# Optimization experiments

Measured on AMD Instinct MI355X. Metric: run time of the kernel, lower is better.

## Reference

```python
import jax, jax.numpy as jnp
import numpy as np

BN_EPS = 1e-5
LEAKY_SLOPE = 0.2


def setup_inputs() -> dict:
    key = jax.random.key(0)
    k1, k2 = jax.random.split(key, 2)
    B, C, N, O, K = 8, 64, 4096, 64, 20
    x = jax.random.normal(k1, (B, C, N), dtype=jnp.float32)
    W = jax.random.normal(k2, (O, 2 * C), dtype=jnp.float32) * 0.05  # 1x1 conv weight
    gamma = jnp.ones((O,), dtype=jnp.float32)
    beta = jnp.zeros((O,), dtype=jnp.float32)
    return {"x": x, "W": W, "gamma": gamma, "beta": beta, "k": K}


def reference(x, W, gamma, beta, k):
    # x: (B, C, N)
    xt = jnp.transpose(x, (0, 2, 1))  # (B, N, C)
    # kNN via squared euclidean distances (same ordering as cdist p=2)
    sq = jnp.sum(xt * xt, axis=-1)  # (B, N)
    d2 = sq[:, :, None] + sq[:, None, :] - 2.0 * jnp.einsum('bnc,bmc->bnm', xt, xt)
    idx = jax.lax.top_k(-d2, k)[1]  # (B, N, k) nearest neighbors (incl. self)
    # gather neighbor features: (B, N, k, C)
    xj = jax.vmap(lambda f, i: f[i])(xt, idx)
    xi = xt[:, :, None, :]  # (B, N, 1, C)
    edge = jnp.concatenate([xj - xi, jnp.broadcast_to(xi, xj.shape)], axis=-1)  # (B, N, k, 2C)
    # 1x1 conv == channel GEMM
    h = jnp.einsum('bnkc,oc->bnko', edge, W)  # (B, N, k, O)
    # BatchNorm2d, training-mode batch statistics over (B, N, k) per channel
    mean = jnp.mean(h, axis=(0, 1, 2))
    var = jnp.mean(jnp.square(h - mean), axis=(0, 1, 2))
    hn = (h - mean) * jax.lax.rsqrt(var + BN_EPS) * gamma + beta
    # LeakyReLU(0.2); dropout omitted (eval / identity)
    act = jnp.where(hn >= 0, hn, LEAKY_SLOPE * hn)
    # max over the k neighbors -> (B, N, O) -> (B, O, N)
    out = jnp.max(act, axis=2)
    return jnp.transpose(out, (0, 2, 1))
```

## Files before the change

### kernel.cpp

```cpp
#include <hip/hip_runtime.h>
#include <math.h>

#define Bn 8
#define Cc 64
#define Nn 4096
#define Oo 64
#define Kk 20
#define Kh 10
#define QCAP 16
#define NTOT (Bn*Nn*Kk)

typedef __attribute__((ext_vector_type(8))) short short8;
typedef __attribute__((ext_vector_type(4))) float f32x4;

__device__ __forceinline__ unsigned bf16_rn(float v) {
  unsigned u = __float_as_uint(v);
  return (u + 0x7FFFu + ((u >> 16) & 1)) >> 16;
}

__global__ __launch_bounds__(256) void k_split(const float* __restrict__ x,
                                               unsigned short* __restrict__ xs3,
                                               float* __restrict__ sqv) {
  __shared__ float xs[64][68];
  int tid = threadIdx.x;
  int b = blockIdx.x & 7;
  int n0 = (blockIdx.x >> 3) << 6;
  for (int i = 0; i < 4; i++) {
    int c = i * 16 + (tid >> 4);
    int n = (tid & 15) * 4;
    float4 v = *(const float4*)&x[((size_t)b * Cc + c) * Nn + n0 + n];
    *(float4*)&xs[c][n] = v;
  }
  __syncthreads();
  for (int i = 0; i < 4; i++) {
    int n = i * 16 + (tid >> 4);
    int c = (tid & 15) * 4;
    ushort4 h4, m4, l4;
    unsigned short* hp = (unsigned short*)&h4;
    unsigned short* mp = (unsigned short*)&m4;
    unsigned short* lp = (unsigned short*)&l4;
#pragma unroll
    for (int j = 0; j < 4; j++) {
      float v = xs[c + j][n];
      unsigned hb = bf16_rn(v);
      float hf = __uint_as_float(hb << 16);
      float r1 = v - hf;
      unsigned mb = bf16_rn(r1);
      float mf = __uint_as_float(mb << 16);
      float r2 = r1 - mf;
      unsigned lb = bf16_rn(r2);
      hp[j] = (unsigned short)hb;
      mp[j] = (unsigned short)mb;
      lp[j] = (unsigned short)lb;
    }
    size_t o = ((size_t)(b << 12) + n0 + n) * 192 + c;
    *(ushort4*)&xs3[o] = h4;
    *(ushort4*)&xs3[o + 64] = m4;
    *(ushort4*)&xs3[o + 128] = l4;
  }
  if (tid < 64) {
    float s = 0.f;
#pragma unroll
    for (int c = 0; c < 64; c++) { float v = xs[c][tid]; s = fmaf(v, v, s); }
    sqv[b * Nn + n0 + tid] = s;
  }
}

__global__ __launch_bounds__(256) void k_y1z(const float* __restrict__ x,
                                             const float* __restrict__ Wm,
                                             float* __restrict__ y1,
                                             float* __restrict__ z) {
  __shared__ float xs[64][68];
  __shared__ float Wl[64][129];
  int tid = threadIdx.x;
  int b = blockIdx.x & 7;
  int n0 = (blockIdx.x >> 3) << 6;
  for (int i = tid; i < 64 * 128; i += 256) Wl[i >> 7][i & 127] = Wm[i];
  for (int i = 0; i < 4; i++) {
    int c = i * 16 + (tid >> 4);
    int n = (tid & 15) * 4;
    float4 v = *(const float4*)&x[((size_t)b * Cc + c) * Nn + n0 + n];
    *(float4*)&xs[c][n] = v;
  }
  __syncthreads();
  int o = tid & 63, ng = tid >> 6;
  for (int p = 0; p < 4; p++) {
    int nb = p * 16 + ng * 4;
    float a1[4] = {0.f, 0.f, 0.f, 0.f};
    float a2[4] = {0.f, 0.f, 0.f, 0.f};
#pragma unroll 8
    for (int c = 0; c < 64; c++) {
      float4 xv = *(const float4*)&xs[c][nb];
      float w1v = Wl[o][c], w2v = Wl[o][64 + c];
      float xa[4] = {xv.x, xv.y, xv.z, xv.w};
#pragma unroll
      for (int j = 0; j < 4; j++) {
        a1[j] = fmaf(xa[j], w1v, a1[j]);
        a2[j] = fmaf(xa[j], w2v, a2[j]);
      }
    }
#pragma unroll
    for (int j = 0; j < 4; j++) {
      size_t off = ((size_t)b * Nn + n0 + nb + j) * 64 + o;
      y1[off] = a1[j];
      z[off] = a2[j] - a1[j];
    }
  }
}

__global__ __launch_bounds__(512, 4) void k_knn(const unsigned short* __restrict__ xs3,
                                                const float* __restrict__ sqv,
                                                int* __restrict__ idxout) {
  __shared__ alignas(16) short Bs[2][3][64][72];
  __shared__ float thrS[2][64];
  __shared__ float sqs[2][64];
  __shared__ alignas(16) float qk[2][64][20];
  __shared__ alignas(16) unsigned short qm[2][64][24];
  __shared__ int qcnt[2][64];

  const int tid = threadIdx.x;
  const int lane = tid & 63;
  const int w = tid >> 6;
  const int grp = w >> 2;
  const int wg = w & 3;
  const int tig = tid & 255;
  const int b = blockIdx.x & 7;
  const int n0 = (blockIdx.x >> 3) << 6;
  const int lm = lane & 15;
  const int q = lane >> 4;
  const bool handler = (lane < 32);
  const int hrow = wg * 16 + (lane >> 1);
  const bool isL = (lane & 1) == 0;

  float hk[Kh];
  int hix[Kh];
#pragma unroll
  for (int kk = 0; kk < Kh; kk++) { hk[kk] = INFINITY; hix[kk] = 0; }

  if (handler && !isL) { thrS[grp][hrow] = INFINITY; qcnt[grp][hrow] = 0; }

  const size_t arow = ((size_t)(b << 12) + n0 + wg * 16 + lm) * 192;
  short8 ah0 = *(const short8*)&xs3[arow + q * 8];
  short8 ah1 = *(const short8*)&xs3[arow + 32 + q * 8];
  short8 am0 = *(const short8*)&xs3[arow + 64 + q * 8];
  short8 am1 = *(const short8*)&xs3[arow + 96 + q * 8];
  short8 al0 = *(const short8*)&xs3[arow + 128 + q * 8];
  short8 al1 = *(const short8*)&xs3[arow + 160 + q * 8];

  const unsigned short* gp = xs3 + ((size_t)(b << 12) + grp * 2048) * 192 + tig * 8;
  short* ld[6];
#pragma unroll
  for (int i = 0; i < 6; i++) {
    int f = i * 256 + tig;
    int r = f / 24;
    int rem = f - r * 24;
    int layer = rem >> 3;
    int qq = rem & 7;
    ld[i] = &Bs[grp][layer][r][qq * 8];
  }

  f32x4 acc[4];

  for (int t = 0; t < 32; t++) {
    const int m0 = grp * 2048 + t * 64;
    __syncthreads();
#pragma unroll
    for (int i = 0; i < 6; i++) {
      short8 v = *(const short8*)(gp + i * 2048);
      *(short8*)ld[i] = v;
    }
    gp += 12288;
    if (tig < 16) ((float4*)sqs[grp])[tig] = ((const float4*)(sqv + b * Nn + m0))[tig];
    __syncthreads();

#pragma unroll
    for (int g = 0; g < 4; g++) {
      const int mr = g * 16 + lm;
      short8 bh0 = *(const short8*)&Bs[grp][0][mr][q * 8];
      short8 bh1 = *(const short8*)&Bs[grp][0][mr][32 + q * 8];
      short8 bm0 = *(const short8*)&Bs[grp][1][mr][q * 8];
      short8 bm1 = *(const short8*)&Bs[grp][1][mr][32 + q * 8];
      short8 bl0 = *(const short8*)&Bs[grp][2][mr][q * 8];
      short8 bl1 = *(const short8*)&Bs[grp][2][mr][32 + q * 8];
      f32x4 a = (f32x4){0.f, 0.f, 0.f, 0.f};
      a = __builtin_amdgcn_mfma_f32_16x16x32_bf16(am0, bm0, a, 0, 0, 0);
      a = __builtin_amdgcn_mfma_f32_16x16x32_bf16(am1, bm1, a, 0, 0, 0);
      a = __builtin_amdgcn_mfma_f32_16x16x32_bf16(ah0, bl0, a, 0, 0, 0);
      a = __builtin_amdgcn_mfma_f32_16x16x32_bf16(ah1, bl1, a, 0, 0, 0);
      a = __builtin_amdgcn_mfma_f32_16x16x32_bf16(al0, bh0, a, 0, 0, 0);
      a = __builtin_amdgcn_mfma_f32_16x16x32_bf16(al1, bh1, a, 0, 0, 0);
      a = __builtin_amdgcn_mfma_f32_16x16x32_bf16(ah0, bm0, a, 0, 0, 0);
      a = __builtin_amdgcn_mfma_f32_16x16x32_bf16(ah1, bm1, a, 0, 0, 0);
      a = __builtin_amdgcn_mfma_f32_16x16x32_bf16(am0, bh0, a, 0, 0, 0);
      a = __builtin_amdgcn_mfma_f32_16x16x32_bf16(am1, bh1, a, 0, 0, 0);
      a = __builtin_amdgcn_mfma_f32_16x16x32_bf16(ah0, bh0, a, 0, 0, 0);
      a = __builtin_amdgcn_mfma_f32_16x16x32_bf16(ah1, bh1, a, 0, 0, 0);
      acc[g] = a;
    }

    unsigned pend = 0;
    {
      float tl[4];
#pragma unroll
      for (int r = 0; r < 4; r++) tl[r] = thrS[grp][wg * 16 + q * 4 + r];
#pragma unroll
      for (int g = 0; g < 4; g++) {
        float sv = sqs[grp][g * 16 + lm];
#pragma unroll
        for (int r = 0; r < 4; r++) {
          float key = fmaf(-2.f, acc[g][r], sv);
          acc[g][r] = key;
          if (key < tl[r]) pend |= 1u << (g * 4 + r);
        }
      }
    }

    for (;;) {
      if (pend) {
#pragma unroll
        for (int g = 0; g < 4; g++) {
#pragma unroll
          for (int r = 0; r < 4; r++) {
            unsigned bit = 1u << (g * 4 + r);
            if (pend & bit) {
              int row = wg * 16 + q * 4 + r;
              int p = atomicAdd(&qcnt[grp][row], 1);
              if (p < QCAP) {
                qk[grp][row][p] = acc[g][r];
                qm[grp][row][p] = (unsigned short)(m0 + g * 16 + lm);
                pend &= ~bit;
              }
            }
          }
        }
      }
      unsigned long long anyovf = __ballot(pend != 0);

      if (handler) {
        int cn = qcnt[grp][hrow];
        if (cn > QCAP) cn = QCAP;
        for (int p0 = 0; p0 < cn; p0 += 4) {
          float4 kv4 = *(const float4*)&qk[grp][hrow][p0];
          ushort4 mv4 = *(const ushort4*)&qm[grp][hrow][p0];
          float kva[4] = {kv4.x, kv4.y, kv4.z, kv4.w};
          unsigned short mva[4] = {mv4.x, mv4.y, mv4.z, mv4.w};
#pragma unroll
          for (int j = 0; j < 4; j++) {
            bool valid = (p0 + j < cn);
            float kv = kva[j];
            int ki = (int)mva[j];
            bool lins = kv < hk[Kh - 1];
            float pv = lins ? hk[Kh - 1] : kv;
            int pi = lins ? hix[Kh - 1] : ki;
            float rv = __shfl_xor(pv, 1);
            int ri = __shfl_xor(pi, 1);
            float mval = isL ? kv : rv;
            int midx = isL ? ki : ri;
            if (valid && mval < hk[Kh - 1]) {
              bool cm[Kh];
#pragma unroll
              for (int kk = 0; kk < Kh; kk++) cm[kk] = mval < hk[kk];
#pragma unroll
              for (int kk = Kh - 1; kk >= 1; kk--) {
                hk[kk]  = cm[kk] ? (cm[kk - 1] ? hk[kk - 1]  : mval) : hk[kk];
                hix[kk] = cm[kk] ? (cm[kk - 1] ? hix[kk - 1] : midx) : hix[kk];
              }
              if (cm[0]) { hk[0] = mval; hix[0] = midx; }
            }
          }
        }
        if (cn && !isL) { qcnt[grp][hrow] = 0; thrS[grp][hrow] = hk[Kh - 1]; }
      }
      if (!anyovf) break;
      if (pend) {
        float tl[4];
#pragma unroll
        for (int r = 0; r < 4; r++) tl[r] = thrS[grp][wg * 16 + q * 4 + r];
#pragma unroll
        for (int g = 0; g < 4; g++)
#pragma unroll
          for (int r = 0; r < 4; r++) {
            unsigned bit = 1u << (g * 4 + r);
            if ((pend & bit) && acc[g][r] >= tl[r]) pend &= ~bit;
          }
      }
    }
  }

  if (grp == 1 && handler) {
    int base = isL ? 0 : Kh;
#pragma unroll
    for (int kk = 0; kk < Kh; kk++) {
      qk[1][hrow][base + kk] = hk[kk];
      qm[1][hrow][base + kk] = (unsigned short)hix[kk];
    }
  }
  __syncthreads();
  if (grp == 0 && handler) {
    for (int p0 = 0; p0 < Kk; p0 += 4) {
      float4 kv4 = *(const float4*)&qk[1][hrow][p0];
      ushort4 mv4 = *(const ushort4*)&qm[1][hrow][p0];
      float kva[4] = {kv4.x, kv4.y, kv4.z, kv4.w};
      unsigned short mva[4] = {mv4.x, mv4.y, mv4.z, mv4.w};
#pragma unroll
      for (int j = 0; j < 4; j++) {
        float kv = kva[j];
        int ki = (int)mva[j];
        bool lins = kv < hk[Kh - 1];
        float pv = lins ? hk[Kh - 1] : kv;
        int pi = lins ? hix[Kh - 1] : ki;
        float rv = __shfl_xor(pv, 1);
        int ri = __shfl_xor(pi, 1);
        float mval = isL ? kv : rv;
        int midx = isL ? ki : ri;
        if (mval < hk[Kh - 1]) {
          bool cm[Kh];
#pragma unroll
          for (int kk = 0; kk < Kh; kk++) cm[kk] = mval < hk[kk];
#pragma unroll
          for (int kk = Kh - 1; kk >= 1; kk--) {
            hk[kk]  = cm[kk] ? (cm[kk - 1] ? hk[kk - 1]  : mval) : hk[kk];
            hix[kk] = cm[kk] ? (cm[kk - 1] ? hix[kk - 1] : midx) : hix[kk];
          }
          if (cm[0]) { hk[0] = mval; hix[0] = midx; }
        }
      }
    }
    size_t obase = ((size_t)b * Nn + n0 + hrow) * Kk + (isL ? 0 : Kh);
#pragma unroll
    for (int kk = 0; kk < Kh; kk++) idxout[obase + kk] = hix[kk];
  }
}

__global__ __launch_bounds__(256) void k_stats(const float* __restrict__ y1,
                                               const float* __restrict__ z,
                                               const int* __restrict__ idxp,
                                               float* __restrict__ parts) {
  __shared__ float rs[4][64];
  __shared__ float rq[4][64];
  int tid = threadIdx.x;
  int o = tid & 63, g = tid >> 6;
  int b = blockIdx.x & 7;
  int n0 = (blockIdx.x >> 3) << 6;
  const float* y1b = y1 + (size_t)b * Nn * 64;
  float s = 0.f, ss = 0.f;
  for (int t = 0; t < 16; t++) {
    int n = n0 + g + t * 4;
    size_t base = (size_t)b * Nn + n;
    float zv = z[base * 64 + o];
    const int* ip = idxp + base * Kk;
#pragma unroll
    for (int k = 0; k < Kk; k++) {
      int j = ip[k];
      float hv = y1b[(size_t)j * 64 + o] + zv;
      s += hv;
      ss = fmaf(hv, hv, ss);
    }
  }
  rs[g][o] = s;
  rq[g][o] = ss;
  __syncthreads();
  if (tid < 64) {
    parts[(size_t)blockIdx.x * 128 + tid] = rs[0][tid] + rs[1][tid] + rs[2][tid] + rs[3][tid];
    parts[(size_t)blockIdx.x * 128 + 64 + tid] = rq[0][tid] + rq[1][tid] + rq[2][tid] + rq[3][tid];
  }
}

__global__ __launch_bounds__(128) void k_reduce(const float* __restrict__ parts,
                                                float* __restrict__ stats) {
  int tid = threadIdx.x;
  float s = 0.f;
  for (int i = 0; i < 512; i += 4) {
    s += parts[(size_t)i * 128 + tid] + parts[(size_t)(i + 1) * 128 + tid] +
         parts[(size_t)(i + 2) * 128 + tid] + parts[(size_t)(i + 3) * 128 + tid];
  }
  stats[tid] = s;
}

__global__ __launch_bounds__(256) void k_out(const float* __restrict__ y1,
                                             const float* __restrict__ z,
                                             const int* __restrict__ idxp,
                                             const float* __restrict__ stats,
                                             const float* __restrict__ gamma,
                                             const float* __restrict__ beta,
                                             float* __restrict__ out) {
  __shared__ float T[64][65];
  int tid = threadIdx.x;
  int lane = tid & 63;
  int w = tid >> 6;
  int b = blockIdx.x & 7;
  int n0 = (blockIdx.x >> 3) << 6;
  int o = lane;
  const float inv = 1.0f / (float)NTOT;
  float mean = stats[o] * inv;
  float var = fmaf(-mean, mean, stats[64 + o] * inv);
  float sc = gamma[o] * rsqrtf(var + 1e-5f);
  float bi = fmaf(-mean, sc, beta[o]);
  const float* y1b = y1 + (size_t)b * Nn * 64;
  for (int t = 0; t < 16; t++) {
    int nl = w + t * 4;
    size_t base = (size_t)b * Nn + n0 + nl;
    float zv = z[base * 64 + o];
    const int* ip = idxp + base * Kk;
    float mv = -INFINITY;
#pragma unroll
    for (int k = 0; k < Kk; k++) {
      int j = ip[k];
      float hv = y1b[(size_t)j * 64 + o] + zv;
      float hn = fmaf(hv, sc, bi);
      float a = (hn >= 0.f) ? hn : 0.2f * hn;
      mv = fmaxf(mv, a);
    }
    T[o][nl] = mv;
  }
  __syncthreads();
  for (int t = 0; t < 16; t++) {
    int oo = w * 16 + t;
    out[((size_t)b * Oo + oo) * Nn + n0 + lane] = T[oo][lane];
  }
}

extern "C" void kernel_launch(void* const* d_in, const int* in_sizes, int n_in,
                              void* d_out, int out_size, void* d_ws, size_t ws_size,
                              hipStream_t stream) {
  const float* x = (const float*)d_in[0];
  const float* W = (const float*)d_in[1];
  const float* gamma = (const float*)d_in[2];
  const float* beta = (const float*)d_in[3];

  char* ws = (char*)d_ws;
  unsigned short* xs3 = (unsigned short*)ws;
  float* y1 = (float*)ws;
  float* z = (float*)(ws + 8388608);
  float* sq = (float*)(ws + 16777216);
  float* stats = (float*)(ws + 16908288);
  int* idx = (int*)(ws + 16908800);
  float* parts = (float*)(ws + 19530240);
  float* out = (float*)d_out;

  k_split<<<Bn * (Nn / 64), 256, 0, stream>>>(x, xs3, sq);
  k_knn<<<Bn * (Nn / 64), 512, 0, stream>>>(xs3, sq, idx);
  k_y1z<<<Bn * (Nn / 64), 256, 0, stream>>>(x, W, y1, z);
  k_stats<<<Bn * (Nn / 64), 256, 0, stream>>>(y1, z, idx, parts);
  k_reduce<<<1, 128, 0, stream>>>(parts, stats);
  k_out<<<Bn * (Nn / 64), 256, 0, stream>>>(y1, z, idx, stats, gamma, beta, out);
}
```

Measured before the change: 384.3 us.

## Split per-row top-k across lane quads with DPP cascade and swizzled LDS

Each query row's top-20 list is now held by four lanes with five entries each instead of two lanes with ten, and candidates cascade between lanes through DPP quad permutes. All 64 lanes now do insertion work rather than only 32. The B tile in LDS moves to a flat XOR-swizzled layout to reduce bank conflicts. The second half-group also prunes candidates against the first group's threshold, and the queue capacity grows to 24. The cascade makes the insertion logic harder to follow and adds more cross-lane exchanges per candidate.

```diff
diff --git a/kernel.cpp b/kernel.cpp
--- a/kernel.cpp
+++ b/kernel.cpp
@@ -6,8 +6,8 @@
 #define Nn 4096
 #define Oo 64
 #define Kk 20
-#define Kh 10
-#define QCAP 16
+#define Kq 5
+#define QCAP 24
 #define NTOT (Bn*Nn*Kk)
 
 typedef __attribute__((ext_vector_type(8))) short short8;
@@ -16,6 +16,38 @@
 __device__ __forceinline__ unsigned bf16_rn(float v) {
   unsigned u = __float_as_uint(v);
   return (u + 0x7FFFu + ((u >> 16) & 1)) >> 16;
+}
+
+template <int P>
+__device__ __forceinline__ float qperm_f(float v) {
+  return __int_as_float(__builtin_amdgcn_mov_dpp(__float_as_int(v), P, 0xF, 0xF, true));
+}
+template <int P>
+__device__ __forceinline__ int qperm_i(int v) {
+  return __builtin_amdgcn_mov_dpp(v, P, 0xF, 0xF, true);
+}
+
+__device__ __forceinline__ void quad_insert(float (&hk)[Kq], int (&hix)[Kq],
+                                            float kv, int ki, int dj, bool valid) {
+  float lmax = hk[4];
+  int lmi = hix[4];
+  float t1 = qperm_f<0x90>(lmax); int i1 = qperm_i<0x90>(lmi);
+  float t2 = qperm_f<0x40>(lmax); int i2 = qperm_i<0x40>(lmi);
+  float t3 = qperm_f<0x00>(lmax); int i3 = qperm_i<0x00>(lmi);
+  float e = t3; int ei = i3;
+  if (t2 > e) { e = t2; ei = i2; }
+  if (t1 > e) { e = t1; ei = i1; }
+  bool useE = (dj != 0) && (e > kv);
+  float in = useE ? e : kv;
+  int ii = useE ? ei : ki;
+  if (valid && in < hk[4]) {
+    bool c0 = in < hk[0], c1 = in < hk[1], c2 = in < hk[2], c3 = in < hk[3];
+    hk[4] = c3 ? hk[3] : in;                hix[4] = c3 ? hix[3] : ii;
+    hk[3] = c3 ? (c2 ? hk[2] : in) : hk[3]; hix[3] = c3 ? (c2 ? hix[2] : ii) : hix[3];
+    hk[2] = c2 ? (c1 ? hk[1] : in) : hk[2]; hix[2] = c2 ? (c1 ? hix[1] : ii) : hix[2];
+    hk[1] = c1 ? (c0 ? hk[0] : in) : hk[1]; hix[1] = c1 ? (c0 ? hix[0] : ii) : hix[1];
+    if (c0) { hk[0] = in; hix[0] = ii; }
+  }
 }
 
 __global__ __launch_bounds__(256) void k_split(const float* __restrict__ x,
@@ -111,11 +143,11 @@
 __global__ __launch_bounds__(512, 4) void k_knn(const unsigned short* __restrict__ xs3,
                                                 const float* __restrict__ sqv,
                                                 int* __restrict__ idxout) {
-  __shared__ alignas(16) short Bs[2][3][64][72];
-  __shared__ float thrS[2][64];
-  __shared__ float sqs[2][64];
-  __shared__ alignas(16) float qk[2][64][20];
-  __shared__ alignas(16) unsigned short qm[2][64][24];
+  __shared__ alignas(16) short Bs[2][12288];
+  __shared__ alignas(16) float thrS[2][64];
+  __shared__ alignas(16) float sqs[2][64];
+  __shared__ alignas(16) float qk[2][64][QCAP];
+  __shared__ alignas(16) unsigned short qm[2][64][QCAP];
   __shared__ int qcnt[2][64];
 
   const int tid = threadIdx.x;
@@ -128,16 +160,16 @@
   const int n0 = (blockIdx.x >> 3) << 6;
   const int lm = lane & 15;
   const int q = lane >> 4;
-  const bool handler = (lane < 32);
-  const int hrow = wg * 16 + (lane >> 1);
-  const bool isL = (lane & 1) == 0;
-
-  float hk[Kh];
-  int hix[Kh];
-#pragma unroll
-  for (int kk = 0; kk < Kh; kk++) { hk[kk] = INFINITY; hix[kk] = 0; }
-
-  if (handler && !isL) { thrS[grp][hrow] = INFINITY; qcnt[grp][hrow] = 0; }
+  const int rowq = wg * 16 + q * 4;
+  const int drow = wg * 16 + (lane >> 2);
+  const int dj = lane & 3;
+
+  float hk[Kq];
+  int hix[Kq];
+#pragma unroll
+  for (int kk = 0; kk < Kq; kk++) { hk[kk] = INFINITY; hix[kk] = 0; }
+
+  if (dj == 3) { thrS[grp][drow] = INFINITY; qcnt[grp][drow] = 0; }
 
   const size_t arow = ((size_t)(b << 12) + n0 + wg * 16 + lm) * 192;
   short8 ah0 = *(const short8*)&xs3[arow + q * 8];
@@ -153,11 +185,11 @@
   for (int i = 0; i < 6; i++) {
     int f = i * 256 + tig;
     int r = f / 24;
-    int rem = f - r * 24;
-    int layer = rem >> 3;
-    int qq = rem & 7;
-    ld[i] = &Bs[grp][layer][r][qq * 8];
-  }
+    ld[i] = &Bs[grp][(f * 8) ^ ((r & 7) << 3)];
+  }
+  const int qa = ((q ^ (lm & 7)) << 3);
+  const int qb = (((q + 4) ^ (lm & 7)) << 3);
+  const short* Bg = &Bs[grp][0];
 
   f32x4 acc[4];
 
@@ -175,13 +207,13 @@
 
 #pragma unroll
     for (int g = 0; g < 4; g++) {
-      const int mr = g * 16 + lm;
-      short8 bh0 = *(const short8*)&Bs[grp][0][mr][q * 8];
-      short8 bh1 = *(const short8*)&Bs[grp][0][mr][32 + q * 8];
-      short8 bm0 = *(const short8*)&Bs[grp][1][mr][q * 8];
-      short8 bm1 = *(const short8*)&Bs[grp][1][mr][32 + q * 8];
-      short8 bl0 = *(const short8*)&Bs[grp][2][mr][q * 8];
-      short8 bl1 = *(const short8*)&Bs[grp][2][mr][32 + q * 8];
+      const short* brow = Bg + (g * 16 + lm) * 192;
+      short8 bh0 = *(const short8*)(brow + qa);
+      short8 bh1 = *(const short8*)(brow + qb);
+      short8 bm0 = *(const short8*)(brow + 64 + qa);
+      short8 bm1 = *(const short8*)(brow + 64 + qb);
+      short8 bl0 = *(const short8*)(brow + 128 + qa);
+      short8 bl1 = *(const short8*)(brow + 128 + qb);
       f32x4 a = (f32x4){0.f, 0.f, 0.f, 0.f};
       a = __builtin_amdgcn_mfma_f32_16x16x32_bf16(am0, bm0, a, 0, 0, 0);
       a = __builtin_amdgcn_mfma_f32_16x16x32_bf16(am1, bm1, a, 0, 0, 0);
@@ -200,9 +232,13 @@
 
     unsigned pend = 0;
     {
-      float tl[4];
-#pragma unroll
-      for (int r = 0; r < 4; r++) tl[r] = thrS[grp][wg * 16 + q * 4 + r];
+      float4 t4 = *(const float4*)&thrS[grp][rowq];
+      float tl[4] = {t4.x, t4.y, t4.z, t4.w};
+      if (grp) {
+        float4 s4 = *(const float4*)&thrS[0][rowq];
+        tl[0] = fminf(tl[0], s4.x); tl[1] = fminf(tl[1], s4.y);
+        tl[2] = fminf(tl[2], s4.z); tl[3] = fminf(tl[3], s4.w);
+      }
 #pragma unroll
       for (int g = 0; g < 4; g++) {
         float sv = sqs[grp][g * 16 + lm];
@@ -223,7 +259,7 @@
           for (int r = 0; r < 4; r++) {
             unsigned bit = 1u << (g * 4 + r);
             if (pend & bit) {
-              int row = wg * 16 + q * 4 + r;
+              int row = rowq + r;
               int p = atomicAdd(&qcnt[grp][row], 1);
               if (p < QCAP) {
                 qk[grp][row][p] = acc[g][r];
@@ -236,46 +272,26 @@
       }
       unsigned long long anyovf = __ballot(pend != 0);
 
-      if (handler) {
-        int cn = qcnt[grp][hrow];
+      {
+        int cn = qcnt[grp][drow];
         if (cn > QCAP) cn = QCAP;
-        for (int p0 = 0; p0 < cn; p0 += 4) {
-          float4 kv4 = *(const float4*)&qk[grp][hrow][p0];
-          ushort4 mv4 = *(const ushort4*)&qm[grp][hrow][p0];
-          float kva[4] = {kv4.x, kv4.y, kv4.z, kv4.w};
-          unsigned short mva[4] = {mv4.x, mv4.y, mv4.z, mv4.w};
-#pragma unroll
-          for (int j = 0; j < 4; j++) {
-            bool valid = (p0 + j < cn);
-            float kv = kva[j];
-            int ki = (int)mva[j];
-            bool lins = kv < hk[Kh - 1];
-            float pv = lins ? hk[Kh - 1] : kv;
-            int pi = lins ? hix[Kh - 1] : ki;
-            float rv = __shfl_xor(pv, 1);
-            int ri = __shfl_xor(pi, 1);
-            float mval = isL ? kv : rv;
-            int midx = isL ? ki : ri;
-            if (valid && mval < hk[Kh - 1]) {
-              bool cm[Kh];
-#pragma unroll
-              for (int kk = 0; kk < Kh; kk++) cm[kk] = mval < hk[kk];
-#pragma unroll
-              for (int kk = Kh - 1; kk >= 1; kk--) {
-                hk[kk]  = cm[kk] ? (cm[kk - 1] ? hk[kk - 1]  : mval) : hk[kk];
-                hix[kk] = cm[kk] ? (cm[kk - 1] ? hix[kk - 1] : midx) : hix[kk];
-              }
-              if (cm[0]) { hk[0] = mval; hix[0] = midx; }
-            }
-          }
+        for (int p0 = 0; p0 < cn; p0 += 2) {
+          float2 kv2 = *(const float2*)&qk[grp][drow][p0];
+          ushort2 mv2 = *(const ushort2*)&qm[grp][drow][p0];
+          quad_insert(hk, hix, kv2.x, (int)mv2.x, dj, true);
+          quad_insert(hk, hix, kv2.y, (int)mv2.y, dj, p0 + 1 < cn);
         }
-        if (cn && !isL) { qcnt[grp][hrow] = 0; thrS[grp][hrow] = hk[Kh - 1]; }
+        if (cn && dj == 3) { qcnt[grp][drow] = 0; thrS[grp][drow] = hk[4]; }
       }
       if (!anyovf) break;
       if (pend) {
-        float tl[4];
-#pragma unroll
-        for (int r = 0; r < 4; r++) tl[r] = thrS[grp][wg * 16 + q * 4 + r];
+        float4 t4 = *(const float4*)&thrS[grp][rowq];
+        float tl[4] = {t4.x, t4.y, t4.z, t4.w};
+        if (grp) {
+          float4 s4 = *(const float4*)&thrS[0][rowq];
+          tl[0] = fminf(tl[0], s4.x); tl[1] = fminf(tl[1], s4.y);
+          tl[2] = fminf(tl[2], s4.z); tl[3] = fminf(tl[3], s4.w);
+        }
 #pragma unroll
         for (int g = 0; g < 4; g++)
 #pragma unroll
@@ -287,48 +303,24 @@
     }
   }
 
-  if (grp == 1 && handler) {
-    int base = isL ? 0 : Kh;
-#pragma unroll
-    for (int kk = 0; kk < Kh; kk++) {
-      qk[1][hrow][base + kk] = hk[kk];
-      qm[1][hrow][base + kk] = (unsigned short)hix[kk];
+  if (grp == 1) {
+#pragma unroll
+    for (int kk = 0; kk < Kq; kk++) {
+      qk[1][drow][dj * Kq + kk] = hk[kk];
+      qm[1][drow][dj * Kq + kk] = (unsigned short)hix[kk];
     }
   }
   __syncthreads();
-  if (grp == 0 && handler) {
-    for (int p0 = 0; p0 < Kk; p0 += 4) {
-      float4 kv4 = *(const float4*)&qk[1][hrow][p0];
-      ushort4 mv4 = *(const ushort4*)&qm[1][hrow][p0];
-      float kva[4] = {kv4.x, kv4.y, kv4.z, kv4.w};
-      unsigned short mva[4] = {mv4.x, mv4.y, mv4.z, mv4.w};
-#pragma unroll
-      for (int j = 0; j < 4; j++) {
-        float kv = kva[j];
-        int ki = (int)mva[j];
-        bool lins = kv < hk[Kh - 1];
-        float pv = lins ? hk[Kh - 1] : kv;
-        int pi = lins ? hix[Kh - 1] : ki;
-        float rv = __shfl_xor(pv, 1);
-        int ri = __shfl_xor(pi, 1);
-        float mval = isL ? kv : rv;
-        int midx = isL ? ki : ri;
-        if (mval < hk[Kh - 1]) {
-          bool cm[Kh];
-#pragma unroll
-          for (int kk = 0; kk < Kh; kk++) cm[kk] = mval < hk[kk];
-#pragma unroll
-          for (int kk = Kh - 1; kk >= 1; kk--) {
-            hk[kk]  = cm[kk] ? (cm[kk - 1] ? hk[kk - 1]  : mval) : hk[kk];
-            hix[kk] = cm[kk] ? (cm[kk - 1] ? hix[kk - 1] : midx) : hix[kk];
-          }
-          if (cm[0]) { hk[0] = mval; hix[0] = midx; }
-        }
-      }
-    }
-    size_t obase = ((size_t)b * Nn + n0 + hrow) * Kk + (isL ? 0 : Kh);
-#pragma unroll
-    for (int kk = 0; kk < Kh; kk++) idxout[obase + kk] = hix[kk];
+  if (grp == 0) {
+    for (int p0 = 0; p0 < Kk; p0 += 2) {
+      float2 kv2 = *(const float2*)&qk[1][drow][p0];
+      ushort2 mv2 = *(const ushort2*)&qm[1][drow][p0];
+      quad_insert(hk, hix, kv2.x, (int)mv2.x, dj, true);
+      quad_insert(hk, hix, kv2.y, (int)mv2.y, dj, true);
+    }
+    size_t obase = ((size_t)b * Nn + n0 + drow) * Kk + dj * Kq;
+#pragma unroll
+    for (int kk = 0; kk < Kq; kk++) idxout[obase + kk] = hix[kk];
   }
 }
 
```

After: 495.6 us. +29.0%, slower.
